# Performance work log

Hardware: AMD Instinct MI355X
Metric: run time of the kernel (lower is better)

Reference implementation:

```python
import jax, jax.numpy as jnp
import numpy as np

N_HEADS = 16
EMBED_DIM = 1024
HEAD_DIM = EMBED_DIM // N_HEADS
SEQ_LEN = 2048


def setup_inputs() -> dict:
    key = jax.random.key(0)
    ks = jax.random.split(key, 9)
    s = 1.0 / np.sqrt(EMBED_DIM)
    inp = {
        "x": jax.random.normal(ks[0], (SEQ_LEN, EMBED_DIM), dtype=jnp.float32),
        "Wq": jax.random.uniform(ks[1], (EMBED_DIM, EMBED_DIM), jnp.float32, -s, s),
        "bq": jax.random.uniform(ks[2], (EMBED_DIM,), jnp.float32, -s, s),
        "Wk": jax.random.uniform(ks[3], (EMBED_DIM, EMBED_DIM), jnp.float32, -s, s),
        "bk": jax.random.uniform(ks[4], (EMBED_DIM,), jnp.float32, -s, s),
        "Wv": jax.random.uniform(ks[5], (EMBED_DIM, EMBED_DIM), jnp.float32, -s, s),
        "bv": jax.random.uniform(ks[6], (EMBED_DIM,), jnp.float32, -s, s),
        "Wo": jax.random.uniform(ks[7], (EMBED_DIM, EMBED_DIM), jnp.float32, -s, s),
        "bo": jax.random.uniform(ks[8], (EMBED_DIM,), jnp.float32, -s, s),
    }
    return inp


def reference(x, Wq, bq, Wk, bk, Wv, bv, Wo, bo):
    # Linear layers (torch convention: y = x @ W.T + b)
    Q = x @ Wq.T + bq  # [S, E]
    K = x @ Wk.T + bk
    V = x @ Wv.T + bv
    # split heads -> [H, S, D]
    def split(t):
        return t.reshape(SEQ_LEN, N_HEADS, HEAD_DIM).transpose(1, 0, 2)
    Qh, Kh, Vh = split(Q), split(K), split(V)
    # NOTE: faithful to source, scale is sqrt(embed_dim), not sqrt(head_dim)
    scale = 1.0 / np.sqrt(EMBED_DIM)
    scores = jnp.einsum("hsd,htd->hst", Qh, Kh) * scale  # [H, S, S]
    attn = jax.nn.softmax(scores, axis=-1)
    ctx = jnp.einsum("hst,htd->hsd", attn, Vh)  # [H, S, D]
    ctx = ctx.transpose(1, 0, 2).reshape(SEQ_LEN, EMBED_DIM)
    out = ctx @ Wo.T + bo
    return (out, attn)
```

## Files before the change

### kernel.cpp

```cpp
#include <hip/hip_runtime.h>
#include <hip/hip_bf16.h>
#include <stdint.h>

#define SQL 2048
#define EMB 1024
#define NHD 16
#define HDD 64

typedef __bf16 bf16x8 __attribute__((ext_vector_type(8)));
typedef __bf16 bf16x4 __attribute__((ext_vector_type(4)));
typedef float f32x4 __attribute__((ext_vector_type(4)));

__device__ __forceinline__ f32x4 mfma16(bf16x8 a, bf16x8 b, f32x4 c) {
    return __builtin_amdgcn_mfma_f32_16x16x32_bf16(a, b, c, 0, 0, 0);
}

__device__ __forceinline__ void gload_lds16(const __bf16* g, __bf16* lds) {
    __builtin_amdgcn_global_load_lds(
        (const __attribute__((address_space(1))) uint32_t*)g,
        (__attribute__((address_space(3))) uint32_t*)lds,
        16, 0, 0);
}

__global__ void cast_bf16_kernel(const float* __restrict__ in, __bf16* __restrict__ out, int n4) {
    int i = blockIdx.x * blockDim.x + threadIdx.x;
    if (i >= n4) return;
    float4 v = ((const float4*)in)[i];
    bf16x4 o;
    o[0] = (__bf16)v.x; o[1] = (__bf16)v.y; o[2] = (__bf16)v.z; o[3] = (__bf16)v.w;
    ((bf16x4*)out)[i] = o;
}

template<bool OUT_BF16>
__global__ __launch_bounds__(256, 2)
void gemm_bt(const __bf16* __restrict__ A,
             const __bf16* __restrict__ B0, const __bf16* __restrict__ B1, const __bf16* __restrict__ B2,
             const float* __restrict__ bias0, const float* __restrict__ bias1, const float* __restrict__ bias2,
             void* __restrict__ out0, void* __restrict__ out1, void* __restrict__ out2,
             float s0, float s1, float s2,
             int M, int N, int K)
{
    const __bf16* B = B0; const float* bias = bias0; void* Cout = out0; float cscale = s0;
    if (blockIdx.z == 1) { B = B1; bias = bias1; Cout = out1; cscale = s1; }
    if (blockIdx.z == 2) { B = B2; bias = bias2; Cout = out2; cscale = s2; }

    __shared__ __attribute__((aligned(16))) __bf16 As[128 * 32];
    __shared__ __attribute__((aligned(16))) __bf16 Bs[128 * 32];

    const int tid  = threadIdx.x;
    const int lane = tid & 63;
    const int wave = tid >> 6;
    const int lrow = lane & 15;
    const int quad = lane >> 4;
    const int bm = blockIdx.y * 128;
    const int bn = blockIdx.x * 128;
    const int wm = (wave >> 1) * 64;
    const int wn = (wave & 1) * 64;

    const f32x4 fzero = {0.f, 0.f, 0.f, 0.f};
    f32x4 acc[4][4];
#pragma unroll
    for (int i = 0; i < 4; i++)
#pragma unroll
        for (int j = 0; j < 4; j++) acc[i][j] = fzero;

    const int srow = (lane >> 2);
    const int scol = (lane & 3) * 8;

    for (int k0 = 0; k0 < K; k0 += 32) {
        __syncthreads();
#pragma unroll
        for (int i = 0; i < 2; i++) {
            int rbase = wave * 32 + i * 16;
            gload_lds16(&A[(size_t)(bm + rbase + srow) * K + k0 + scol], &As[rbase * 32]);
            gload_lds16(&B[(size_t)(bn + rbase + srow) * K + k0 + scol], &Bs[rbase * 32]);
        }
        __syncthreads();
        bf16x8 af[4], bfr[4];
#pragma unroll
        for (int i = 0; i < 4; i++) af[i]  = *(const bf16x8*)&As[(wm + i * 16 + lrow) * 32 + quad * 8];
#pragma unroll
        for (int i = 0; i < 4; i++) bfr[i] = *(const bf16x8*)&Bs[(wn + i * 16 + lrow) * 32 + quad * 8];
#pragma unroll
        for (int mi = 0; mi < 4; mi++)
#pragma unroll
            for (int ni = 0; ni < 4; ni++)
                acc[mi][ni] = mfma16(af[mi], bfr[ni], acc[mi][ni]);
    }

#pragma unroll
    for (int mi = 0; mi < 4; mi++) {
        int row = bm + wm + mi * 16 + quad * 4;
#pragma unroll
        for (int ni = 0; ni < 4; ni++) {
            int col = bn + wn + ni * 16 + lrow;
            float bv = bias[col];
#pragma unroll
            for (int r = 0; r < 4; r++) {
                float v = (acc[mi][ni][r] + bv) * cscale;
                if (OUT_BF16) ((__bf16*)Cout)[(size_t)(row + r) * N + col] = (__bf16)v;
                else          ((float*)Cout)[(size_t)(row + r) * N + col] = v;
            }
        }
    }
}

__global__ __launch_bounds__(256, 2)
void transpose_v(const __bf16* __restrict__ V, __bf16* __restrict__ Vt) {
    __shared__ __attribute__((aligned(16))) __bf16 tile[64][72];
    const int tid = threadIdx.x;
    const int s0 = blockIdx.x * 64;
    const int c0 = blockIdx.y * 64;
#pragma unroll
    for (int i = 0; i < 2; i++) {
        int lin = tid + i * 256;
        int r  = lin >> 3;
        int cg = (lin & 7) << 3;
        *(bf16x8*)&tile[r][cg] = *(const bf16x8*)&V[(size_t)(s0 + r) * EMB + c0 + cg];
    }
    __syncthreads();
#pragma unroll
    for (int i = 0; i < 2; i++) {
        int lin = tid + i * 256;
        int c  = lin >> 3;
        int sg = (lin & 7) << 3;
        bf16x8 t;
#pragma unroll
        for (int j = 0; j < 8; j++) t[j] = tile[sg + j][c];
        *(bf16x8*)&Vt[(size_t)(c0 + c) * SQL + s0 + sg] = t;
    }
}

__global__ __launch_bounds__(256, 2)
void attn_kernel(const __bf16* __restrict__ Qg, const __bf16* __restrict__ Kg,
                 const __bf16* __restrict__ Vt, float* __restrict__ attn,
                 __bf16* __restrict__ ctx)
{
    __shared__ __attribute__((aligned(16))) __bf16 Ks[64][72];
    __shared__ __attribute__((aligned(16))) __bf16 Vs[64][72];
    __shared__ __attribute__((aligned(16))) __bf16 Ps[4][16][72];

    const int tid  = threadIdx.x;
    const int lane = tid & 63;
    const int w    = tid >> 6;
    const int lrow = lane & 15;
    const int quad = lane >> 4;
    const int h  = blockIdx.y;
    const int q0 = blockIdx.x * 64;
    const f32x4 fzero = {0.f, 0.f, 0.f, 0.f};

    const size_t qoff = (size_t)(q0 + w * 16 + lrow) * EMB + h * HDD;
    const bf16x8 qf0 = *(const bf16x8*)&Qg[qoff + quad * 8];
    const bf16x8 qf1 = *(const bf16x8*)&Qg[qoff + 32 + quad * 8];

    float m = -1e30f, l = 0.f;

    for (int k0 = 0; k0 < SQL; k0 += 64) {
        __syncthreads();
#pragma unroll
        for (int i = 0; i < 2; i++) {
            int lin = tid + i * 256;
            int r  = lin >> 3;
            int cg = (lin & 7) << 3;
            *(bf16x8*)&Ks[r][cg] = *(const bf16x8*)&Kg[(size_t)(k0 + r) * EMB + h * HDD + cg];
        }
        __syncthreads();
        f32x4 st[4];
#pragma unroll
        for (int nt = 0; nt < 4; nt++) {
            bf16x8 b0 = *(const bf16x8*)&Ks[nt * 16 + lrow][quad * 8];
            bf16x8 b1 = *(const bf16x8*)&Ks[nt * 16 + lrow][32 + quad * 8];
            f32x4 a = mfma16(b0, qf0, fzero);
            a = mfma16(b1, qf1, a);
            st[nt] = a;
        }
        float tm = -1e30f;
#pragma unroll
        for (int nt = 0; nt < 4; nt++)
#pragma unroll
            for (int r = 0; r < 4; r++) tm = fmaxf(tm, st[nt][r]);
        tm = fmaxf(tm, __shfl_xor(tm, 16));
        tm = fmaxf(tm, __shfl_xor(tm, 32));
        float mn = fmaxf(m, tm);
        float rs = 0.f;
#pragma unroll
        for (int nt = 0; nt < 4; nt++)
#pragma unroll
            for (int r = 0; r < 4; r++) rs += __expf(st[nt][r] - mn);
        rs += __shfl_xor(rs, 16);
        rs += __shfl_xor(rs, 32);
        l = l * __expf(m - mn) + rs;
        m = mn;
    }

    const float rinv = 1.f / l;

    f32x4 o[4];
#pragma unroll
    for (int nt = 0; nt < 4; nt++) o[nt] = fzero;

    float* __restrict__ arow = attn + (size_t)h * SQL * SQL + (size_t)(q0 + w * 16 + lrow) * SQL;

    for (int k0 = 0; k0 < SQL; k0 += 64) {
        __syncthreads();
#pragma unroll
        for (int i = 0; i < 2; i++) {
            int lin = tid + i * 256;
            int r  = lin >> 3;
            int cg = (lin & 7) << 3;
            *(bf16x8*)&Ks[r][cg] = *(const bf16x8*)&Kg[(size_t)(k0 + r) * EMB + h * HDD + cg];
            *(bf16x8*)&Vs[r][cg] = *(const bf16x8*)&Vt[(size_t)(h * HDD + r) * SQL + k0 + cg];
        }
        __syncthreads();
#pragma unroll
        for (int nt = 0; nt < 4; nt++) {
            bf16x8 b0 = *(const bf16x8*)&Ks[nt * 16 + lrow][quad * 8];
            bf16x8 b1 = *(const bf16x8*)&Ks[nt * 16 + lrow][32 + quad * 8];
            f32x4 a = mfma16(b0, qf0, fzero);
            a = mfma16(b1, qf1, a);
            f32x4 pv;
            bf16x4 pb;
#pragma unroll
            for (int r = 0; r < 4; r++) {
                float p = __expf(a[r] - m) * rinv;
                pv[r] = p;
                pb[r] = (__bf16)p;
            }
            *(f32x4*)&arow[k0 + nt * 16 + quad * 4] = pv;
            *(bf16x4*)&Ps[w][lrow][nt * 16 + quad * 4] = pb;
        }
        bf16x8 pf0 = *(const bf16x8*)&Ps[w][lrow][quad * 8];
        bf16x8 pf1 = *(const bf16x8*)&Ps[w][lrow][32 + quad * 8];
#pragma unroll
        for (int nt = 0; nt < 4; nt++) {
            bf16x8 v0 = *(const bf16x8*)&Vs[nt * 16 + lrow][quad * 8];
            bf16x8 v1 = *(const bf16x8*)&Vs[nt * 16 + lrow][32 + quad * 8];
            o[nt] = mfma16(pf0, v0, o[nt]);
            o[nt] = mfma16(pf1, v1, o[nt]);
        }
    }

#pragma unroll
    for (int nt = 0; nt < 4; nt++)
#pragma unroll
        for (int r = 0; r < 4; r++)
            ctx[(size_t)(q0 + w * 16 + quad * 4 + r) * EMB + h * HDD + nt * 16 + lrow] = (__bf16)o[nt][r];
}

extern "C" void kernel_launch(void* const* d_in, const int* in_sizes, int n_in,
                              void* d_out, int out_size, void* d_ws, size_t ws_size,
                              hipStream_t stream)
{
    const float* x  = (const float*)d_in[0];
    const float* Wq = (const float*)d_in[1];
    const float* bq = (const float*)d_in[2];
    const float* Wk = (const float*)d_in[3];
    const float* bk = (const float*)d_in[4];
    const float* Wv = (const float*)d_in[5];
    const float* bv = (const float*)d_in[6];
    const float* Wo = (const float*)d_in[7];
    const float* bo = (const float*)d_in[8];

    float* out  = (float*)d_out;
    float* attn = out + (size_t)SQL * EMB;

    const size_t M1 = 1u << 20;
    __bf16* wsb = (__bf16*)d_ws;
    __bf16* xb  = wsb;
    __bf16* wqb = wsb + 2 * M1;
    __bf16* wkb = wsb + 3 * M1;
    __bf16* wvb = wsb + 4 * M1;
    __bf16* wob = wsb + 5 * M1;
    __bf16* Qb  = wsb + 6 * M1;
    __bf16* Kb  = wsb + 8 * M1;
    __bf16* Vb  = wsb + 10 * M1;
    __bf16* Vtb = wsb + 12 * M1;
    __bf16* ctb = wsb + 14 * M1;

    cast_bf16_kernel<<<(SQL * EMB / 4 + 255) / 256, 256, 0, stream>>>(x,  xb,  SQL * EMB / 4);
    cast_bf16_kernel<<<(EMB * EMB / 4 + 255) / 256, 256, 0, stream>>>(Wq, wqb, EMB * EMB / 4);
    cast_bf16_kernel<<<(EMB * EMB / 4 + 255) / 256, 256, 0, stream>>>(Wk, wkb, EMB * EMB / 4);
    cast_bf16_kernel<<<(EMB * EMB / 4 + 255) / 256, 256, 0, stream>>>(Wv, wvb, EMB * EMB / 4);
    cast_bf16_kernel<<<(EMB * EMB / 4 + 255) / 256, 256, 0, stream>>>(Wo, wob, EMB * EMB / 4);

    gemm_bt<true><<<dim3(EMB / 128, SQL / 128, 3), 256, 0, stream>>>(
        xb, wqb, wkb, wvb, bq, bk, bv,
        (void*)Qb, (void*)Kb, (void*)Vb,
        0.03125f, 1.0f, 1.0f, SQL, EMB, EMB);

    transpose_v<<<dim3(SQL / 64, EMB / 64), 256, 0, stream>>>(Vb, Vtb);

    attn_kernel<<<dim3(SQL / 64, NHD), 256, 0, stream>>>(Qb, Kb, Vtb, attn, ctb);

    gemm_bt<false><<<dim3(EMB / 128, SQL / 128, 1), 256, 0, stream>>>(
        ctb, wob, wob, wob, bo, bo, bo,
        (void*)out, (void*)out, (void*)out,
        1.0f, 1.0f, 1.0f, SQL, EMB, EMB);
}
```

Measured before the change: 409.5 us.

## Split attention keys across warps with LDS merge; fuse five cast launches

Result: slower. 424.8 us (+3.7%).

```diff
diff --git a/kernel.cpp b/kernel.cpp
--- a/kernel.cpp
+++ b/kernel.cpp
@@ -22,10 +22,18 @@
         16, 0, 0);
 }
 
-__global__ void cast_bf16_kernel(const float* __restrict__ in, __bf16* __restrict__ out, int n4) {
+__global__ void cast5_kernel(const float* __restrict__ x, const float* __restrict__ wq,
+                             const float* __restrict__ wk, const float* __restrict__ wv,
+                             const float* __restrict__ wo, __bf16* __restrict__ out)
+{
     int i = blockIdx.x * blockDim.x + threadIdx.x;
-    if (i >= n4) return;
-    float4 v = ((const float4*)in)[i];
+    const float* src; int off;
+    if      (i < (512 << 10))  { src = x;  off = 0; }
+    else if (i < (768 << 10))  { src = wq; off = 512 << 10; }
+    else if (i < (1024 << 10)) { src = wk; off = 768 << 10; }
+    else if (i < (1280 << 10)) { src = wv; off = 1024 << 10; }
+    else                       { src = wo; off = 1280 << 10; }
+    float4 v = ((const float4*)src)[i - off];
     bf16x4 o;
     o[0] = (__bf16)v.x; o[1] = (__bf16)v.y; o[2] = (__bf16)v.z; o[3] = (__bf16)v.w;
     ((bf16x4*)out)[i] = o;
@@ -136,115 +144,154 @@
                  const __bf16* __restrict__ Vt, float* __restrict__ attn,
                  __bf16* __restrict__ ctx)
 {
-    __shared__ __attribute__((aligned(16))) __bf16 Ks[64][72];
-    __shared__ __attribute__((aligned(16))) __bf16 Vs[64][72];
-    __shared__ __attribute__((aligned(16))) __bf16 Ps[4][16][72];
+    __shared__ __attribute__((aligned(16))) __bf16 Ps[4][32][40];
+    __shared__ float MLb[2][2][2][16][2];
+    __shared__ float Ored[64][66];
 
     const int tid  = threadIdx.x;
     const int lane = tid & 63;
     const int w    = tid >> 6;
+    const int wq   = w & 1;
+    const int wk   = w >> 1;
     const int lrow = lane & 15;
     const int quad = lane >> 4;
     const int h  = blockIdx.y;
     const int q0 = blockIdx.x * 64;
     const f32x4 fzero = {0.f, 0.f, 0.f, 0.f};
 
-    const size_t qoff = (size_t)(q0 + w * 16 + lrow) * EMB + h * HDD;
-    const bf16x8 qf0 = *(const bf16x8*)&Qg[qoff + quad * 8];
-    const bf16x8 qf1 = *(const bf16x8*)&Qg[qoff + 32 + quad * 8];
-
-    float m = -1e30f, l = 0.f;
+    bf16x8 qf[2][2];
+#pragma unroll
+    for (int qg = 0; qg < 2; qg++) {
+        const size_t qoff = (size_t)(q0 + wq * 32 + qg * 16 + lrow) * EMB + h * HDD;
+        qf[qg][0] = *(const bf16x8*)&Qg[qoff + quad * 8];
+        qf[qg][1] = *(const bf16x8*)&Qg[qoff + 32 + quad * 8];
+    }
+
+    float m[2] = {-1e30f, -1e30f}, l[2] = {0.f, 0.f};
 
     for (int k0 = 0; k0 < SQL; k0 += 64) {
-        __syncthreads();
-#pragma unroll
-        for (int i = 0; i < 2; i++) {
-            int lin = tid + i * 256;
-            int r  = lin >> 3;
-            int cg = (lin & 7) << 3;
-            *(bf16x8*)&Ks[r][cg] = *(const bf16x8*)&Kg[(size_t)(k0 + r) * EMB + h * HDD + cg];
-        }
-        __syncthreads();
-        f32x4 st[4];
-#pragma unroll
-        for (int nt = 0; nt < 4; nt++) {
-            bf16x8 b0 = *(const bf16x8*)&Ks[nt * 16 + lrow][quad * 8];
-            bf16x8 b1 = *(const bf16x8*)&Ks[nt * 16 + lrow][32 + quad * 8];
-            f32x4 a = mfma16(b0, qf0, fzero);
-            a = mfma16(b1, qf1, a);
-            st[nt] = a;
-        }
-        float tm = -1e30f;
+        f32x4 st[2][2];
+#pragma unroll
+        for (int kt = 0; kt < 2; kt++) {
+            const __bf16* kp = &Kg[(size_t)(k0 + wk * 32 + kt * 16 + lrow) * EMB + h * HDD];
+            bf16x8 b0 = *(const bf16x8*)&kp[quad * 8];
+            bf16x8 b1 = *(const bf16x8*)&kp[32 + quad * 8];
+#pragma unroll
+            for (int qg = 0; qg < 2; qg++) {
+                f32x4 a = mfma16(b0, qf[qg][0], fzero);
+                st[qg][kt] = mfma16(b1, qf[qg][1], a);
+            }
+        }
+#pragma unroll
+        for (int qg = 0; qg < 2; qg++) {
+            float tm = -1e30f;
+#pragma unroll
+            for (int kt = 0; kt < 2; kt++)
+#pragma unroll
+                for (int r = 0; r < 4; r++) tm = fmaxf(tm, st[qg][kt][r]);
+            tm = fmaxf(tm, __shfl_xor(tm, 16));
+            tm = fmaxf(tm, __shfl_xor(tm, 32));
+            float mn = fmaxf(m[qg], tm);
+            float rs = 0.f;
+#pragma unroll
+            for (int kt = 0; kt < 2; kt++)
+#pragma unroll
+                for (int r = 0; r < 4; r++) rs += __expf(st[qg][kt][r] - mn);
+            rs += __shfl_xor(rs, 16);
+            rs += __shfl_xor(rs, 32);
+            l[qg] = l[qg] * __expf(m[qg] - mn) + rs;
+            m[qg] = mn;
+        }
+    }
+
+    if (quad == 0) {
+#pragma unroll
+        for (int qg = 0; qg < 2; qg++) {
+            MLb[wk][wq][qg][lrow][0] = m[qg];
+            MLb[wk][wq][qg][lrow][1] = l[qg];
+        }
+    }
+    __syncthreads();
+    float rinv[2];
+#pragma unroll
+    for (int qg = 0; qg < 2; qg++) {
+        float mo = MLb[wk ^ 1][wq][qg][lrow][0];
+        float lo = MLb[wk ^ 1][wq][qg][lrow][1];
+        float mf = fmaxf(m[qg], mo);
+        float lf = l[qg] * __expf(m[qg] - mf) + lo * __expf(mo - mf);
+        m[qg] = mf;
+        rinv[qg] = 1.f / lf;
+    }
+
+    f32x4 o[2][4];
+#pragma unroll
+    for (int qg = 0; qg < 2; qg++)
+#pragma unroll
+        for (int nt = 0; nt < 4; nt++) o[qg][nt] = fzero;
+
+    float* arow[2];
+#pragma unroll
+    for (int qg = 0; qg < 2; qg++)
+        arow[qg] = attn + (size_t)h * SQL * SQL + (size_t)(q0 + wq * 32 + qg * 16 + lrow) * SQL;
+
+    for (int k0 = 0; k0 < SQL; k0 += 64) {
+        bf16x8 vf[4];
 #pragma unroll
         for (int nt = 0; nt < 4; nt++)
-#pragma unroll
-            for (int r = 0; r < 4; r++) tm = fmaxf(tm, st[nt][r]);
-        tm = fmaxf(tm, __shfl_xor(tm, 16));
-        tm = fmaxf(tm, __shfl_xor(tm, 32));
-        float mn = fmaxf(m, tm);
-        float rs = 0.f;
+            vf[nt] = *(const bf16x8*)&Vt[(size_t)(h * HDD + nt * 16 + lrow) * SQL + k0 + wk * 32 + quad * 8];
+
+#pragma unroll
+        for (int kt = 0; kt < 2; kt++) {
+            const __bf16* kp = &Kg[(size_t)(k0 + wk * 32 + kt * 16 + lrow) * EMB + h * HDD];
+            bf16x8 b0 = *(const bf16x8*)&kp[quad * 8];
+            bf16x8 b1 = *(const bf16x8*)&kp[32 + quad * 8];
+#pragma unroll
+            for (int qg = 0; qg < 2; qg++) {
+                f32x4 a = mfma16(b0, qf[qg][0], fzero);
+                a = mfma16(b1, qf[qg][1], a);
+                f32x4 pv; bf16x4 pb;
+#pragma unroll
+                for (int r = 0; r < 4; r++) {
+                    float p = __expf(a[r] - m[qg]) * rinv[qg];
+                    pv[r] = p; pb[r] = (__bf16)p;
+                }
+                *(f32x4*)&arow[qg][k0 + wk * 32 + kt * 16 + quad * 4] = pv;
+                *(bf16x4*)&Ps[w][qg * 16 + lrow][kt * 16 + quad * 4] = pb;
+            }
+        }
+        bf16x8 pf[2];
+#pragma unroll
+        for (int qg = 0; qg < 2; qg++)
+            pf[qg] = *(const bf16x8*)&Ps[w][qg * 16 + lrow][quad * 8];
 #pragma unroll
         for (int nt = 0; nt < 4; nt++)
 #pragma unroll
-            for (int r = 0; r < 4; r++) rs += __expf(st[nt][r] - mn);
-        rs += __shfl_xor(rs, 16);
-        rs += __shfl_xor(rs, 32);
-        l = l * __expf(m - mn) + rs;
-        m = mn;
-    }
-
-    const float rinv = 1.f / l;
-
-    f32x4 o[4];
-#pragma unroll
-    for (int nt = 0; nt < 4; nt++) o[nt] = fzero;
-
-    float* __restrict__ arow = attn + (size_t)h * SQL * SQL + (size_t)(q0 + w * 16 + lrow) * SQL;
-
-    for (int k0 = 0; k0 < SQL; k0 += 64) {
-        __syncthreads();
-#pragma unroll
-        for (int i = 0; i < 2; i++) {
-            int lin = tid + i * 256;
-            int r  = lin >> 3;
-            int cg = (lin & 7) << 3;
-            *(bf16x8*)&Ks[r][cg] = *(const bf16x8*)&Kg[(size_t)(k0 + r) * EMB + h * HDD + cg];
-            *(bf16x8*)&Vs[r][cg] = *(const bf16x8*)&Vt[(size_t)(h * HDD + r) * SQL + k0 + cg];
-        }
-        __syncthreads();
-#pragma unroll
-        for (int nt = 0; nt < 4; nt++) {
-            bf16x8 b0 = *(const bf16x8*)&Ks[nt * 16 + lrow][quad * 8];
-            bf16x8 b1 = *(const bf16x8*)&Ks[nt * 16 + lrow][32 + quad * 8];
-            f32x4 a = mfma16(b0, qf0, fzero);
-            a = mfma16(b1, qf1, a);
-            f32x4 pv;
-            bf16x4 pb;
-#pragma unroll
-            for (int r = 0; r < 4; r++) {
-                float p = __expf(a[r] - m) * rinv;
-                pv[r] = p;
-                pb[r] = (__bf16)p;
-            }
-            *(f32x4*)&arow[k0 + nt * 16 + quad * 4] = pv;
-            *(bf16x4*)&Ps[w][lrow][nt * 16 + quad * 4] = pb;
-        }
-        bf16x8 pf0 = *(const bf16x8*)&Ps[w][lrow][quad * 8];
-        bf16x8 pf1 = *(const bf16x8*)&Ps[w][lrow][32 + quad * 8];
-#pragma unroll
-        for (int nt = 0; nt < 4; nt++) {
-            bf16x8 v0 = *(const bf16x8*)&Vs[nt * 16 + lrow][quad * 8];
-            bf16x8 v1 = *(const bf16x8*)&Vs[nt * 16 + lrow][32 + quad * 8];
-            o[nt] = mfma16(pf0, v0, o[nt]);
-            o[nt] = mfma16(pf1, v1, o[nt]);
-        }
-    }
-
-#pragma unroll
-    for (int nt = 0; nt < 4; nt++)
-#pragma unroll
-        for (int r = 0; r < 4; r++)
-            ctx[(size_t)(q0 + w * 16 + quad * 4 + r) * EMB + h * HDD + nt * 16 + lrow] = (__bf16)o[nt][r];
+            for (int qg = 0; qg < 2; qg++)
+                o[qg][nt] = mfma16(pf[qg], vf[nt], o[qg][nt]);
+    }
+
+    if (wk == 1) {
+#pragma unroll
+        for (int qg = 0; qg < 2; qg++)
+#pragma unroll
+            for (int nt = 0; nt < 4; nt++)
+#pragma unroll
+                for (int r = 0; r < 4; r++)
+                    Ored[wq * 32 + qg * 16 + quad * 4 + r][nt * 16 + lrow] = o[qg][nt][r];
+    }
+    __syncthreads();
+    if (wk == 0) {
+#pragma unroll
+        for (int qg = 0; qg < 2; qg++)
+#pragma unroll
+            for (int nt = 0; nt < 4; nt++)
+#pragma unroll
+                for (int r = 0; r < 4; r++) {
+                    int qrow = wq * 32 + qg * 16 + quad * 4 + r;
+                    float v = o[qg][nt][r] + Ored[qrow][nt * 16 + lrow];
+                    ctx[(size_t)(q0 + qrow) * EMB + h * HDD + nt * 16 + lrow] = (__bf16)v;
+                }
+    }
 }
 
 extern "C" void kernel_launch(void* const* d_in, const int* in_sizes, int n_in,
@@ -277,11 +324,7 @@
     __bf16* Vtb = wsb + 12 * M1;
     __bf16* ctb = wsb + 14 * M1;
 
-    cast_bf16_kernel<<<(SQL * EMB / 4 + 255) / 256, 256, 0, stream>>>(x,  xb,  SQL * EMB / 4);
-    cast_bf16_kernel<<<(EMB * EMB / 4 + 255) / 256, 256, 0, stream>>>(Wq, wqb, EMB * EMB / 4);
-    cast_bf16_kernel<<<(EMB * EMB / 4 + 255) / 256, 256, 0, stream>>>(Wk, wkb, EMB * EMB / 4);
-    cast_bf16_kernel<<<(EMB * EMB / 4 + 255) / 256, 256, 0, stream>>>(Wv, wvb, EMB * EMB / 4);
-    cast_bf16_kernel<<<(EMB * EMB / 4 + 255) / 256, 256, 0, stream>>>(Wo, wob, EMB * EMB / 4);
+    cast5_kernel<<<6144, 256, 0, stream>>>(x, Wq, Wk, Wv, Wo, wsb);
 
     gemm_bt<true><<<dim3(EMB / 128, SQL / 128, 3), 256, 0, stream>>>(
         xb, wqb, wkb, wvb, bq, bk, bv,
```
